# Kernel tuning notes

Measured on AMD Instinct MI355X. Metric: run time of the kernel, lower is better.

The kernel has to match this reference:

```python
import jax, jax.numpy as jnp
import numpy as np

QDEPTH = 20
WIDTH = HEIGHT = 28
PIXELS = WIDTH * HEIGHT          # 784
WIRES = 10                        # ceil(log2(784))
BATCH = 8192


def setup_inputs() -> dict:
    key = jax.random.key(0)
    k1, k2, k3, k4 = jax.random.split(key, 4)
    x = jax.random.normal(k1, (BATCH, 1, WIDTH, HEIGHT), jnp.float32)
    W = jax.random.normal(k2, (WIRES, PIXELS), jnp.float32) / np.sqrt(PIXELS)
    b = jax.random.normal(k3, (WIRES,), jnp.float32) * 0.01
    qweights = jax.random.normal(k4, (QDEPTH, WIRES, 3), jnp.float32) * 0.4
    return {"x": x, "W": W, "b": b, "qweights": qweights}


def _apply_1q(state, gate, wire):
    """Apply a single-qubit gate. state: (B,)+(2,)*WIRES; gate: (2,2) or (B,2,2)."""
    ax = 1 + wire
    s = jnp.moveaxis(state, ax, 1)
    shp = s.shape
    s = s.reshape(shp[0], 2, -1)
    if gate.ndim == 2:
        s = jnp.einsum('ij,bjr->bir', gate, s)
    else:
        s = jnp.einsum('bij,bjr->bir', gate, s)
    return jnp.moveaxis(s.reshape(shp), 1, ax)


def _cnot(state, c, t):
    """CNOT with control c, target t on state (B,)+(2,)*WIRES."""
    s = jnp.moveaxis(state, (1 + c, 1 + t), (1, 2))
    # when control==1, flip target axis
    s = jnp.concatenate([s[:, :1], jnp.flip(s[:, 1:2], axis=2)], axis=1)
    return jnp.moveaxis(s, (1, 2), (1 + c, 1 + t))


def _ry_batched(theta):
    """theta: (B,) -> (B,2,2) complex RY gates."""
    c = jnp.cos(theta / 2)
    s = jnp.sin(theta / 2)
    g = jnp.stack([jnp.stack([c, -s], -1), jnp.stack([s, c], -1)], -2)
    return g.astype(jnp.complex64)


def _rot(phi, theta, omega):
    """PennyLane Rot(phi,theta,omega) = RZ(omega) RY(theta) RZ(phi), scalars -> (2,2)."""
    c = jnp.cos(theta / 2)
    s = jnp.sin(theta / 2)
    m00 = jnp.exp(-0.5j * (phi + omega)) * c
    m01 = -jnp.exp(0.5j * (phi - omega)) * s
    m10 = jnp.exp(-0.5j * (phi - omega)) * s
    m11 = jnp.exp(0.5j * (phi + omega)) * c
    return jnp.stack([jnp.stack([m00, m01]), jnp.stack([m10, m11])]).astype(jnp.complex64)


def _forward(x, W, b, qweights):
    B = x.shape[0]
    feat = x.reshape(B, -1)                       # b 1 w h -> b (w h)
    angles = feat @ W.T + b                       # linear_down -> (B, WIRES)

    # |0...0> statevector, wire 0 most significant (PennyLane convention)
    state = jnp.zeros((B,) + (2,) * WIRES, jnp.complex64)
    state = state.at[(slice(None),) + (0,) * WIRES].set(1.0)

    # AngleEmbedding, rotation='Y'
    for w in range(WIRES):
        state = _apply_1q(state, _ry_batched(angles[:, w]), w)

    # StronglyEntanglingLayers: per-layer Rot on every wire, then CNOT ring
    for l in range(QDEPTH):
        for w in range(WIRES):
            state = _apply_1q(state, _rot(qweights[l, w, 0], qweights[l, w, 1], qweights[l, w, 2]), w)
        r = (l % (WIRES - 1)) + 1                 # default PennyLane ranges
        for w in range(WIRES):
            state = _cnot(state, w, (w + r) % WIRES)

    sv = state.reshape(B, -1)
    probs = sv.real ** 2 + sv.imag ** 2           # qml.probs over all wires
    out = jnp.clip(probs[:, :PIXELS] * PIXELS, 0.0, 1.0)
    return out.reshape(B, 1, WIDTH, HEIGHT)


def reference(x, W, b, qweights):
    return _forward(x, W, b, qweights)
```

## Files before the change

kernel.cpp:

```cpp
#include <hip/hip_runtime.h>
#include <hip/hip_bf16.h>
#include <stdint.h>


#define NWIRES  10
#define DIM     1024
#define NLAYERS 20
#define NGATES  200
#define NPASS   100
#define PIXELS  784
#define BATCH   8192

typedef _Float16 f16;
typedef _Float16 f16x8 __attribute__((ext_vector_type(8)));
typedef float    f32x4 __attribute__((ext_vector_type(4)));
typedef float    f32x2 __attribute__((ext_vector_type(2)));

typedef const __attribute__((address_space(1))) void* gas1_t;
typedef __attribute__((address_space(3))) void*       las3_t;

__device__ __forceinline__ void gload_lds16(const void* g, void* l) {
  __builtin_amdgcn_global_load_lds((gas1_t)g, (las3_t)l, 16, 0, 0);
}

__global__ __launch_bounds__(256) void k_prep(const float* __restrict__ qw,
                                              float* __restrict__ plan_mat,
                                              unsigned* __restrict__ plan_idx,
                                              unsigned* __restrict__ plan_final) {
  __shared__ float gm[NGATES][8];
  const int tid = threadIdx.x;

  if (tid < NGATES) {
    float phi = qw[tid * 3 + 0], th = qw[tid * 3 + 1], om = qw[tid * 3 + 2];
    float s, c, sa, ca, sb, cb;
    sincosf(0.5f * th, &s, &c);
    sincosf(0.5f * (phi + om), &sa, &ca);
    sincosf(0.5f * (phi - om), &sb, &cb);
    gm[tid][0] = ca * c;  gm[tid][1] = sa * c;
    gm[tid][2] = cb * s;  gm[tid][3] = sb * s;
    gm[tid][4] = -cb * s; gm[tid][5] = sb * s;
    gm[tid][6] = ca * c;  gm[tid][7] = -sa * c;
  }
  __syncthreads();

  if (tid == 0) {
    unsigned rowA[NWIRES], invc[NWIRES];
    for (int i = 0; i < NWIRES; i++) { rowA[i] = 1u << i; invc[i] = 1u << i; }
    for (int lrev = 0; lrev < NLAYERS; lrev++) {
      int l = NLAYERS - 1 - lrev;
      int r = (l % (NWIRES - 1)) + 1;
      for (int w = NWIRES - 1; w >= 0; w--) {
        int c = w, t = (w + r) % NWIRES;
        int pc = 9 - c, pt = 9 - t;
        rowA[pt] ^= rowA[pc];
        invc[pc] ^= invc[pt];
      }
      for (int s = 0; s < 5; s++) {
        int w1 = 2 * s, w2 = 2 * s + 1;
        int p1 = 9 - w1, p2 = 9 - w2;
        unsigned u1 = rowA[p1], u2 = rowA[p2];
        unsigned m1 = invc[p1], m2 = invc[p2];
        unsigned b1 = u1 & (0u - u1);
        if (u2 & b1) u2 ^= u1;
        unsigned b2 = u2 & (0u - u2);
        if (u1 & b2) u1 ^= u2;
        unsigned bLo = (b1 < b2) ? b1 : b2;
        unsigned bHi = (b1 < b2) ? b2 : b1;
        unsigned* P = plan_idx + (size_t)(lrev * 5 + s) * 8;
        P[0] = bLo; P[1] = bHi; P[2] = u1; P[3] = u2;
        P[4] = b1;  P[5] = b2;  P[6] = m1; P[7] = m2;
      }
    }
    for (int p = 0; p < NWIRES; p++) plan_final[p] = invc[p];
  } else if (tid >= 100 && tid < 200) {
    int t = tid - 100;
    int lrev = t / 5, s = t % 5;
    int l = NLAYERS - 1 - lrev;
    int g1 = l * NWIRES + 2 * s, g2 = g1 + 1;
    float* K = plan_mat + (size_t)t * 64;
#pragma unroll
    for (int r = 0; r < 4; r++) {
#pragma unroll
      for (int c = 0; c < 4; c++) {
        int r1 = r >> 1, c1 = c >> 1, r2 = r & 1, c2 = c & 1;
        float ar = gm[g1][(r1 * 2 + c1) * 2], ai = gm[g1][(r1 * 2 + c1) * 2 + 1];
        float br = gm[g2][(r2 * 2 + c2) * 2], bi = gm[g2][(r2 * 2 + c2) * 2 + 1];
        float kr = ar * br - ai * bi;
        float ki = ar * bi + ai * br;
        float* e = K + (r * 4 + c) * 4;
        e[0] = kr; e[1] = kr; e[2] = -ki; e[3] = ki;
      }
    }
  }
}

__global__ __launch_bounds__(256) void k_main(const float* __restrict__ plan_mat,
                                              const unsigned* __restrict__ plan_idx,
                                              const unsigned* __restrict__ plan_final,
                                              const float* __restrict__ x,
                                              const float* __restrict__ W,
                                              const float* __restrict__ bias,
                                              f16* __restrict__ E,
                                              f16* __restrict__ Bt) {
  __shared__ f32x2 st[DIM];
  __shared__ float part[4][NWIRES];
  __shared__ float csh[NWIRES][2];

  const int tid = threadIdx.x;

  if (blockIdx.x < PIXELS) {
    const int col = blockIdx.x;

    for (int i = tid; i < DIM; i += 256)
      st[i] = (f32x2){i == col ? 1.f : 0.f, 0.f};
    __syncthreads();

    for (int t = 0; t < NPASS; t++) {
      const unsigned* P = plan_idx + (size_t)t * 8;
      const unsigned bLo = P[0], bHi = P[1], u1 = P[2], u2 = P[3];
      const unsigned pb1 = P[4], pb2 = P[5], m1 = P[6], m2 = P[7];
      const f32x4* Kp = (const f32x4*)(plan_mat + (size_t)t * 64);

      unsigned q  = (unsigned)tid;
      unsigned xx = ((q & ~(bLo - 1u)) << 1) | (q & (bLo - 1u));
      unsigned j0 = ((xx & ~(bHi - 1u)) << 1) | (xx & (bHi - 1u));
      unsigned j  = j0 ^ ((__popc(u1 & j0) & 1) ? pb1 : 0u)
                       ^ ((__popc(u2 & j0) & 1) ? pb2 : 0u);

      f32x2 v0 = st[j];
      f32x2 v1 = st[j ^ m2];
      f32x2 v2 = st[j ^ m1];
      f32x2 v3 = st[j ^ m1 ^ m2];
      f32x2 w0 = {v0.y, v0.x}, w1 = {v1.y, v1.x};
      f32x2 w2 = {v2.y, v2.x}, w3 = {v3.y, v3.x};

      f32x2 r0 = {0.f, 0.f}, r1 = {0.f, 0.f}, r2 = {0.f, 0.f}, r3 = {0.f, 0.f};
#define CM(rr, e, vv, ww)                         \
      { f32x4 kk = Kp[e];                         \
        rr += (f32x2){kk.x, kk.y} * (vv);         \
        rr += (f32x2){kk.z, kk.w} * (ww); }
      CM(r0, 0, v0, w0)  CM(r0, 1, v1, w1)  CM(r0, 2, v2, w2)  CM(r0, 3, v3, w3)
      CM(r1, 4, v0, w0)  CM(r1, 5, v1, w1)  CM(r1, 6, v2, w2)  CM(r1, 7, v3, w3)
      CM(r2, 8, v0, w0)  CM(r2, 9, v1, w1)  CM(r2, 10, v2, w2) CM(r2, 11, v3, w3)
      CM(r3, 12, v0, w0) CM(r3, 13, v1, w1) CM(r3, 14, v2, w2) CM(r3, 15, v3, w3)
#undef CM

      st[j]           = r0;
      st[j ^ m2]      = r1;
      st[j ^ m1]      = r2;
      st[j ^ m1 ^ m2] = r3;
      __syncthreads();
    }

    unsigned invl[NWIRES];
#pragma unroll
    for (int p = 0; p < NWIRES; p++) invl[p] = plan_final[p];

    __align__(8) f16 re4[4], im4[4];
#pragma unroll
    for (int u = 0; u < 4; u++) {
      int i = tid * 4 + u;
      unsigned j = 0;
#pragma unroll
      for (int p = 0; p < NWIRES; p++)
        if ((i >> p) & 1) j ^= invl[p];
      f32x2 v = st[j];
      re4[u] = (f16)v.x;
      im4[u] = (f16)(-v.y);
    }
    *(uint2*)(&Bt[(size_t)(2 * col) * DIM + tid * 4])     = *(const uint2*)re4;
    *(uint2*)(&Bt[(size_t)(2 * col + 1) * DIM + tid * 4]) = *(const uint2*)im4;
    return;
  }

  const int b = blockIdx.x - PIXELS;
  const float* xr = x + (size_t)b * PIXELS;

  float acc[NWIRES];
#pragma unroll
  for (int w = 0; w < NWIRES; w++) acc[w] = 0.f;

  for (int k = tid; k < PIXELS; k += 256) {
    float xv = xr[k];
#pragma unroll
    for (int w = 0; w < NWIRES; w++) acc[w] = fmaf(xv, W[w * PIXELS + k], acc[w]);
  }

#pragma unroll
  for (int w = 0; w < NWIRES; w++) {
    float v = acc[w];
#pragma unroll
    for (int off = 32; off > 0; off >>= 1) v += __shfl_xor(v, off, 64);
    acc[w] = v;
  }

  const int wv = tid >> 6, ln = tid & 63;
  if (ln == 0) {
#pragma unroll
    for (int w = 0; w < NWIRES; w++) part[wv][w] = acc[w];
  }
  __syncthreads();
  if (tid < NWIRES) {
    float a = part[0][tid] + part[1][tid] + part[2][tid] + part[3][tid] + bias[tid];
    float s, c;
    sincosf(0.5f * a, &s, &c);
    csh[tid][0] = c;
    csh[tid][1] = s;
  }
  __syncthreads();

  __align__(8) f16 e4[4];
#pragma unroll
  for (int u = 0; u < 4; u++) {
    int i = tid * 4 + u;
    float pr = 1.f;
#pragma unroll
    for (int w = 0; w < NWIRES; w++) pr *= csh[w][(i >> (9 - w)) & 1];
    e4[u] = (f16)pr;
  }
  *(uint2*)(&E[(size_t)b * DIM + tid * 4]) = *(const uint2*)e4;
}

__global__ __launch_bounds__(512, 2) void k_gemm(const f16* __restrict__ E,
                                                 const f16* __restrict__ Bt,
                                                 float* __restrict__ out) {
  __shared__ __align__(16) f16 As[4][256 * 32];
  __shared__ __align__(16) f16 Bs[4][256 * 32];

  const int tid = threadIdx.x;
  const int wid = tid >> 6, ln = tid & 63;
  const int wm = wid >> 2, wn = wid & 3;

  const int bid = blockIdx.x;
  const int swz = (bid & 7) * 28 + (bid >> 3);
  const int mt  = swz % 32, nt = swz / 32;
  const int m0  = mt * 256;
  const int n0  = nt * 256;

  f32x4 acc[8][4];
#pragma unroll
  for (int a = 0; a < 8; a++)
#pragma unroll
    for (int q = 0; q < 4; q++) acc[a][q] = (f32x4){0.f, 0.f, 0.f, 0.f};

  int offA[8], offB[4];
#pragma unroll
  for (int mi = 0; mi < 8; mi++) {
    int Ra = wm * 128 + mi * 16 + (ln & 15);
    offA[mi] = Ra * 32 + (((ln >> 4) ^ ((Ra >> 1) & 3)) * 8);
  }
#pragma unroll
  for (int ni = 0; ni < 4; ni++) {
    int Rb = wn * 64 + ni * 16 + (ln & 15);
    offB[ni] = Rb * 32 + (((ln >> 4) ^ ((Rb >> 1) & 3)) * 8);
  }

  auto stage = [&](int t) {
    const int sb = t & 3;
#pragma unroll
    for (int r = 0; r < 2; r++) {
      int u   = r * 512 + tid;
      int row = u >> 2;
      int c16 = (u & 3) ^ ((row >> 1) & 3);
      gload_lds16((const char*)E + (size_t)(m0 + row) * 2048 + t * 64 + c16 * 16,
                  (char*)&As[sb][0] + (size_t)u * 16);
    }
#pragma unroll
    for (int r = 0; r < 2; r++) {
      int u   = r * 512 + tid;
      int row = u >> 2;
      int c16 = (u & 3) ^ ((row >> 1) & 3);
      gload_lds16((const char*)Bt + (size_t)(n0 + row) * 2048 + t * 64 + c16 * 16,
                  (char*)&Bs[sb][0] + (size_t)u * 16);
    }
  };

  stage(0);
  stage(1);
  stage(2);
  asm volatile("s_waitcnt vmcnt(8)" ::: "memory");
  __builtin_amdgcn_s_barrier();

#pragma unroll 4
  for (int k = 0; k < 32; k++) {
    const int buf = k & 3;
    f16x8 af[8], bf[4];
#pragma unroll
    for (int mi = 0; mi < 8; mi++) af[mi] = *(const f16x8*)&As[buf][offA[mi]];
#pragma unroll
    for (int ni = 0; ni < 4; ni++) bf[ni] = *(const f16x8*)&Bs[buf][offB[ni]];

    if (k < 29) stage(k + 3);

    __builtin_amdgcn_s_setprio(1);
#pragma unroll
    for (int mi = 0; mi < 8; mi++)
#pragma unroll
      for (int ni = 0; ni < 4; ni++)
        acc[mi][ni] = __builtin_amdgcn_mfma_f32_16x16x32_f16(
            af[mi], bf[ni], acc[mi][ni], 0, 0, 0);
    __builtin_amdgcn_s_setprio(0);

    if (k < 29)       { asm volatile("s_waitcnt vmcnt(8)" ::: "memory"); }
    else if (k == 29) { asm volatile("s_waitcnt vmcnt(4)" ::: "memory"); }
    else if (k == 30) { asm volatile("s_waitcnt vmcnt(0)" ::: "memory"); }
    __builtin_amdgcn_s_barrier();
  }

#pragma unroll
  for (int mi = 0; mi < 8; mi++) {
#pragma unroll
    for (int ni = 0; ni < 4; ni++) {
      int n = n0 + wn * 64 + ni * 16 + (ln & 15);
      int p = n >> 1;
      bool even = (ln & 1) == 0;
#pragma unroll
      for (int r = 0; r < 4; r++) {
        float v = acc[mi][ni][r];
        float o = __shfl_xor(v, 1, 64);
        if (even && p < PIXELS) {
          int m = m0 + wm * 128 + mi * 16 + (ln >> 4) * 4 + r;
          float s2 = (v * v + o * o) * (float)PIXELS;
          out[(size_t)m * PIXELS + p] = fminf(fmaxf(s2, 0.f), 1.f);
        }
      }
    }
  }
}

extern "C" void kernel_launch(void* const* d_in, const int* in_sizes, int n_in,
                              void* d_out, int out_size, void* d_ws, size_t ws_size,
                              hipStream_t stream) {
  const float* x    = (const float*)d_in[0];
  const float* W    = (const float*)d_in[1];
  const float* bias = (const float*)d_in[2];
  const float* qw   = (const float*)d_in[3];
  float* out        = (float*)d_out;

  char* ws = (char*)d_ws;
  f16* E  = (f16*)(ws);
  f16* Bt = (f16*)(ws + (size_t)16 * 1024 * 1024);
  float*    plan_mat   = (float*)(ws + (size_t)20 * 1024 * 1024);
  unsigned* plan_idx   = (unsigned*)(ws + (size_t)20 * 1024 * 1024 + 65536);
  unsigned* plan_final = (unsigned*)(ws + (size_t)20 * 1024 * 1024 + 131072);

  k_prep<<<dim3(1), dim3(256), 0, stream>>>(qw, plan_mat, plan_idx, plan_final);
  k_main<<<dim3(PIXELS + BATCH), dim3(256), 0, stream>>>(plan_mat, plan_idx,
                                                         plan_final, x, W, bias,
                                                         E, Bt);
  k_gemm<<<dim3(224), dim3(512), 0, stream>>>(E, Bt, out);
}
```

Baseline: 130.5 us.

## Simulate unitary columns per wavefront with fused 4-qubit passes and precomputed indices

Measured after the change: 185.4 us. +42.1%, slower.

```diff
diff --git a/kernel.cpp b/kernel.cpp
--- a/kernel.cpp
+++ b/kernel.cpp
@@ -7,9 +7,9 @@
 #define DIM     1024
 #define NLAYERS 20
 #define NGATES  200
-#define NPASS   100
 #define PIXELS  784
 #define BATCH   8192
+#define NUBLK   196
 
 typedef _Float16 f16;
 typedef _Float16 f16x8 __attribute__((ext_vector_type(8)));
@@ -23,11 +23,25 @@
   __builtin_amdgcn_global_load_lds((gas1_t)g, (las3_t)l, 16, 0, 0);
 }
 
+#define CM(rr, kk, vv)                                  \
+  { f32x4 k_ = (kk);                                    \
+    rr += (f32x2){k_.x, k_.y} * (vv);                   \
+    rr += (f32x2){k_.z, k_.w} * (f32x2){(vv).y, (vv).x}; }
+
 __global__ __launch_bounds__(256) void k_prep(const float* __restrict__ qw,
-                                              float* __restrict__ plan_mat,
-                                              unsigned* __restrict__ plan_idx,
+                                              float* __restrict__ pmatF,
+                                              float* __restrict__ pmatS,
+                                              unsigned* __restrict__ maskF,
+                                              unsigned* __restrict__ maskS,
+                                              unsigned* __restrict__ jtF,
+                                              unsigned* __restrict__ jtS,
                                               unsigned* __restrict__ plan_final) {
-  __shared__ float gm[NGATES][8];
+  __shared__ float    gm[NGATES][8];
+  __shared__ unsigned sF[40][4];
+  __shared__ unsigned sS[20][2];
+  __shared__ unsigned bF[40][8];
+  __shared__ unsigned bS[20][8];
+  __shared__ unsigned tmpR[96][8];
   const int tid = threadIdx.x;
 
   if (tid < NGATES) {
@@ -44,40 +58,40 @@
   __syncthreads();
 
   if (tid == 0) {
-    unsigned rowA[NWIRES], invc[NWIRES];
-    for (int i = 0; i < NWIRES; i++) { rowA[i] = 1u << i; invc[i] = 1u << i; }
+    unsigned rA[NWIRES], ic[NWIRES];
+#pragma unroll
+    for (int i = 0; i < NWIRES; i++) { rA[i] = 1u << i; ic[i] = 1u << i; }
+#pragma unroll
     for (int lrev = 0; lrev < NLAYERS; lrev++) {
-      int l = NLAYERS - 1 - lrev;
-      int r = (l % (NWIRES - 1)) + 1;
+      const int l = NLAYERS - 1 - lrev;
+      const int r = (l % (NWIRES - 1)) + 1;
+#pragma unroll
       for (int w = NWIRES - 1; w >= 0; w--) {
-        int c = w, t = (w + r) % NWIRES;
-        int pc = 9 - c, pt = 9 - t;
-        rowA[pt] ^= rowA[pc];
-        invc[pc] ^= invc[pt];
+        const int c = w, t = (w + r) % NWIRES;
+        rA[9 - t] ^= rA[9 - c];
+        ic[9 - c] ^= ic[9 - t];
       }
-      for (int s = 0; s < 5; s++) {
-        int w1 = 2 * s, w2 = 2 * s + 1;
-        int p1 = 9 - w1, p2 = 9 - w2;
-        unsigned u1 = rowA[p1], u2 = rowA[p2];
-        unsigned m1 = invc[p1], m2 = invc[p2];
-        unsigned b1 = u1 & (0u - u1);
-        if (u2 & b1) u2 ^= u1;
-        unsigned b2 = u2 & (0u - u2);
-        if (u1 & b2) u1 ^= u2;
-        unsigned bLo = (b1 < b2) ? b1 : b2;
-        unsigned bHi = (b1 < b2) ? b2 : b1;
-        unsigned* P = plan_idx + (size_t)(lrev * 5 + s) * 8;
-        P[0] = bLo; P[1] = bHi; P[2] = u1; P[3] = u2;
-        P[4] = b1;  P[5] = b2;  P[6] = m1; P[7] = m2;
-      }
-    }
-    for (int p = 0; p < NWIRES; p++) plan_final[p] = invc[p];
+      sF[2 * lrev][0] = rA[9]; sF[2 * lrev][1] = rA[8];
+      sF[2 * lrev][2] = rA[7]; sF[2 * lrev][3] = rA[6];
+      maskF[(2 * lrev) * 4 + 0] = ic[9]; maskF[(2 * lrev) * 4 + 1] = ic[8];
+      maskF[(2 * lrev) * 4 + 2] = ic[7]; maskF[(2 * lrev) * 4 + 3] = ic[6];
+      sF[2 * lrev + 1][0] = rA[5]; sF[2 * lrev + 1][1] = rA[4];
+      sF[2 * lrev + 1][2] = rA[3]; sF[2 * lrev + 1][3] = rA[2];
+      maskF[(2 * lrev + 1) * 4 + 0] = ic[5]; maskF[(2 * lrev + 1) * 4 + 1] = ic[4];
+      maskF[(2 * lrev + 1) * 4 + 2] = ic[3]; maskF[(2 * lrev + 1) * 4 + 3] = ic[2];
+      sS[lrev][0] = rA[1]; sS[lrev][1] = rA[0];
+      maskS[lrev * 2 + 0] = ic[1]; maskS[lrev * 2 + 1] = ic[0];
+    }
+#pragma unroll
+    for (int p = 0; p < NWIRES; p++) plan_final[p] = ic[p];
   } else if (tid >= 100 && tid < 200) {
     int t = tid - 100;
     int lrev = t / 5, s = t % 5;
     int l = NLAYERS - 1 - lrev;
     int g1 = l * NWIRES + 2 * s, g2 = g1 + 1;
-    float* K = plan_mat + (size_t)t * 64;
+    float* K = (s == 4) ? (pmatS + (size_t)lrev * 64)
+                        : (pmatF + (size_t)(2 * lrev + (s >> 1)) * 128 +
+                           (size_t)(s & 1) * 64);
 #pragma unroll
     for (int r = 0; r < 4; r++) {
 #pragma unroll
@@ -92,88 +106,222 @@
       }
     }
   }
+  __syncthreads();
+
+  if (tid < 40) {
+    unsigned u1 = sF[tid][0], u2 = sF[tid][1], u3 = sF[tid][2], u4 = sF[tid][3];
+    unsigned b1, b2, b3, b4;
+    b1 = u1 & (0u - u1);
+    if (u2 & b1) u2 ^= u1; if (u3 & b1) u3 ^= u1; if (u4 & b1) u4 ^= u1;
+    b2 = u2 & (0u - u2);
+    if (u1 & b2) u1 ^= u2; if (u3 & b2) u3 ^= u2; if (u4 & b2) u4 ^= u2;
+    b3 = u3 & (0u - u3);
+    if (u1 & b3) u1 ^= u3; if (u2 & b3) u2 ^= u3; if (u4 & b3) u4 ^= u3;
+    b4 = u4 & (0u - u4);
+    if (u1 & b4) u1 ^= u4; if (u2 & b4) u2 ^= u4; if (u3 & b4) u3 ^= u4;
+    const unsigned piv = b1 | b2 | b3 | b4;
+    unsigned echPack = 0; int cnt = 0, nrem = 0;
+    for (int f = 0; f < NWIRES; f++) {
+      unsigned ef = 1u << f;
+      if (ef & piv) continue;
+      unsigned v = ef ^ (((u1 >> f) & 1u) ? b1 : 0u)
+                      ^ (((u2 >> f) & 1u) ? b2 : 0u)
+                      ^ (((u3 >> f) & 1u) ? b3 : 0u)
+                      ^ (((u4 >> f) & 1u) ? b4 : 0u);
+      unsigned n = v & 15u;
+#pragma unroll
+      for (int rep = 0; rep < 4; rep++) {
+#pragma unroll
+        for (int k2 = 0; k2 < 4; k2++) {
+          unsigned h = (echPack >> (8 * k2)) & 255u;
+          if (h) { unsigned hb = 0x80000000u >> __clz(h); if (n & hb) n ^= h; }
+        }
+      }
+      if (n && cnt < 4) { echPack |= n << (8 * cnt); bF[tid][cnt] = v; cnt++; }
+      else              { tmpR[tid][nrem] = v; nrem++; }
+    }
+    for (int i = 0; i < nrem; i++) bF[tid][cnt + i] = tmpR[tid][i];
+  } else if (tid >= 64 && tid < 84) {
+    const int lr = tid - 64;
+    unsigned u1 = sS[lr][0], u2 = sS[lr][1];
+    unsigned b1 = u1 & (0u - u1);
+    if (u2 & b1) u2 ^= u1;
+    unsigned b2 = u2 & (0u - u2);
+    if (u1 & b2) u1 ^= u2;
+    const unsigned piv = b1 | b2;
+    unsigned echPack = 0; int cnt = 0, nrem = 0;
+    for (int f = 0; f < NWIRES; f++) {
+      unsigned ef = 1u << f;
+      if (ef & piv) continue;
+      unsigned v = ef ^ (((u1 >> f) & 1u) ? b1 : 0u)
+                      ^ (((u2 >> f) & 1u) ? b2 : 0u);
+      unsigned n = v & 15u;
+#pragma unroll
+      for (int rep = 0; rep < 4; rep++) {
+#pragma unroll
+        for (int k2 = 0; k2 < 4; k2++) {
+          unsigned h = (echPack >> (8 * k2)) & 255u;
+          if (h) { unsigned hb = 0x80000000u >> __clz(h); if (n & hb) n ^= h; }
+        }
+      }
+      if (n && cnt < 4) { echPack |= n << (8 * cnt); bS[lr][cnt] = v; cnt++; }
+      else              { tmpR[tid][nrem] = v; nrem++; }
+    }
+    for (int i = 0; i < nrem; i++) bS[lr][cnt + i] = tmpR[tid][i];
+  }
+  __syncthreads();
+
+  for (int e = tid; e < 40 * 64; e += 256) {
+    int fid = e >> 6, l6 = e & 63;
+    unsigned j = 0;
+#pragma unroll
+    for (int b = 0; b < 6; b++)
+      if ((l6 >> b) & 1) j ^= bF[fid][b];
+    jtF[e] = j;
+  }
+  for (int e = tid; e < 20 * 256; e += 256) {
+    int lr = e >> 8, r8 = e & 255;
+    unsigned j = 0;
+#pragma unroll
+    for (int b = 0; b < 8; b++)
+      if ((r8 >> b) & 1) j ^= bS[lr][b];
+    jtS[e] = j;
+  }
 }
 
-__global__ __launch_bounds__(256) void k_main(const float* __restrict__ plan_mat,
-                                              const unsigned* __restrict__ plan_idx,
+__global__ __launch_bounds__(256) void k_main(const float* __restrict__ pmatF,
+                                              const float* __restrict__ pmatS,
+                                              const unsigned* __restrict__ maskF,
+                                              const unsigned* __restrict__ maskS,
+                                              const unsigned* __restrict__ jtF,
+                                              const unsigned* __restrict__ jtS,
                                               const unsigned* __restrict__ plan_final,
                                               const float* __restrict__ x,
                                               const float* __restrict__ W,
                                               const float* __restrict__ bias,
                                               f16* __restrict__ E,
                                               f16* __restrict__ Bt) {
-  __shared__ f32x2 st[DIM];
+  __shared__ f32x2 st4[4][DIM];
   __shared__ float part[4][NWIRES];
   __shared__ float csh[NWIRES][2];
 
   const int tid = threadIdx.x;
-
-  if (blockIdx.x < PIXELS) {
-    const int col = blockIdx.x;
-
-    for (int i = tid; i < DIM; i += 256)
-      st[i] = (f32x2){i == col ? 1.f : 0.f, 0.f};
-    __syncthreads();
-
-    for (int t = 0; t < NPASS; t++) {
-      const unsigned* P = plan_idx + (size_t)t * 8;
-      const unsigned bLo = P[0], bHi = P[1], u1 = P[2], u2 = P[3];
-      const unsigned pb1 = P[4], pb2 = P[5], m1 = P[6], m2 = P[7];
-      const f32x4* Kp = (const f32x4*)(plan_mat + (size_t)t * 64);
-
-      unsigned q  = (unsigned)tid;
-      unsigned xx = ((q & ~(bLo - 1u)) << 1) | (q & (bLo - 1u));
-      unsigned j0 = ((xx & ~(bHi - 1u)) << 1) | (xx & (bHi - 1u));
-      unsigned j  = j0 ^ ((__popc(u1 & j0) & 1) ? pb1 : 0u)
-                       ^ ((__popc(u2 & j0) & 1) ? pb2 : 0u);
-
-      f32x2 v0 = st[j];
-      f32x2 v1 = st[j ^ m2];
-      f32x2 v2 = st[j ^ m1];
-      f32x2 v3 = st[j ^ m1 ^ m2];
-      f32x2 w0 = {v0.y, v0.x}, w1 = {v1.y, v1.x};
-      f32x2 w2 = {v2.y, v2.x}, w3 = {v3.y, v3.x};
-
-      f32x2 r0 = {0.f, 0.f}, r1 = {0.f, 0.f}, r2 = {0.f, 0.f}, r3 = {0.f, 0.f};
-#define CM(rr, e, vv, ww)                         \
-      { f32x4 kk = Kp[e];                         \
-        rr += (f32x2){kk.x, kk.y} * (vv);         \
-        rr += (f32x2){kk.z, kk.w} * (ww); }
-      CM(r0, 0, v0, w0)  CM(r0, 1, v1, w1)  CM(r0, 2, v2, w2)  CM(r0, 3, v3, w3)
-      CM(r1, 4, v0, w0)  CM(r1, 5, v1, w1)  CM(r1, 6, v2, w2)  CM(r1, 7, v3, w3)
-      CM(r2, 8, v0, w0)  CM(r2, 9, v1, w1)  CM(r2, 10, v2, w2) CM(r2, 11, v3, w3)
-      CM(r3, 12, v0, w0) CM(r3, 13, v1, w1) CM(r3, 14, v2, w2) CM(r3, 15, v3, w3)
-#undef CM
-
-      st[j]           = r0;
-      st[j ^ m2]      = r1;
-      st[j ^ m1]      = r2;
-      st[j ^ m1 ^ m2] = r3;
-      __syncthreads();
+  const int wv = tid >> 6, ln = tid & 63;
+
+  if (blockIdx.x < NUBLK) {
+    const int col = blockIdx.x * 4 + wv;
+    f32x2* st = st4[wv];
+
+#pragma unroll
+    for (int i = 0; i < 16; i++) {
+      int idx = ln + 64 * i;
+      st[idx] = (f32x2){idx == col ? 1.f : 0.f, 0.f};
+    }
+    asm volatile("s_waitcnt lgkmcnt(0)" ::: "memory");
+    __builtin_amdgcn_wave_barrier();
+
+    auto FUSED = [&](int fid, unsigned j) {
+      const unsigned mA1 = maskF[fid * 4 + 0], mA2 = maskF[fid * 4 + 1];
+      const unsigned mB1 = maskF[fid * 4 + 2], mB2 = maskF[fid * 4 + 3];
+      const f32x4* Ka = (const f32x4*)(pmatF + (size_t)fid * 128);
+      const f32x4* Kb = Ka + 16;
+      unsigned ra[4], cb[4];
+      ra[0] = j; ra[1] = j ^ mA2; ra[2] = j ^ mA1; ra[3] = j ^ mA1 ^ mA2;
+      cb[0] = 0; cb[1] = mB2;     cb[2] = mB1;     cb[3] = mB1 ^ mB2;
+      f32x2 v[4][4];
+#pragma unroll
+      for (int ia = 0; ia < 4; ia++)
+#pragma unroll
+        for (int ib = 0; ib < 4; ib++)
+          v[ia][ib] = st[ra[ia] ^ cb[ib]];
+      f32x2 u[4][4];
+#pragma unroll
+      for (int ib = 0; ib < 4; ib++)
+#pragma unroll
+        for (int ia = 0; ia < 4; ia++) {
+          f32x2 acc = {0.f, 0.f};
+#pragma unroll
+          for (int ja = 0; ja < 4; ja++) CM(acc, Ka[ia * 4 + ja], v[ja][ib]);
+          u[ia][ib] = acc;
+        }
+#pragma unroll
+      for (int ia = 0; ia < 4; ia++)
+#pragma unroll
+        for (int ib = 0; ib < 4; ib++) {
+          f32x2 acc = {0.f, 0.f};
+#pragma unroll
+          for (int jb = 0; jb < 4; jb++) CM(acc, Kb[ib * 4 + jb], u[ia][jb]);
+          st[ra[ia] ^ cb[ib]] = acc;
+        }
+      asm volatile("s_waitcnt lgkmcnt(0)" ::: "memory");
+      __builtin_amdgcn_wave_barrier();
+    };
+
+    auto SINGLE = [&](int lay, unsigned j0, unsigned j1, unsigned j2,
+                      unsigned j3) {
+      const unsigned m1 = maskS[lay * 2 + 0], m2 = maskS[lay * 2 + 1];
+      const f32x4* Ks = (const f32x4*)(pmatS + (size_t)lay * 64);
+      unsigned js[4] = {j0, j1, j2, j3};
+#pragma unroll
+      for (int q = 0; q < 4; q++) {
+        unsigned j = js[q];
+        f32x2 v0 = st[j], v1 = st[j ^ m2], v2 = st[j ^ m1], v3 = st[j ^ m1 ^ m2];
+        f32x2 r0 = {0.f, 0.f}, r1 = {0.f, 0.f}, r2 = {0.f, 0.f}, r3 = {0.f, 0.f};
+        CM(r0, Ks[0],  v0) CM(r0, Ks[1],  v1) CM(r0, Ks[2],  v2) CM(r0, Ks[3],  v3)
+        CM(r1, Ks[4],  v0) CM(r1, Ks[5],  v1) CM(r1, Ks[6],  v2) CM(r1, Ks[7],  v3)
+        CM(r2, Ks[8],  v0) CM(r2, Ks[9],  v1) CM(r2, Ks[10], v2) CM(r2, Ks[11], v3)
+        CM(r3, Ks[12], v0) CM(r3, Ks[13], v1) CM(r3, Ks[14], v2) CM(r3, Ks[15], v3)
+        st[j]           = r0;
+        st[j ^ m2]      = r1;
+        st[j ^ m1]      = r2;
+        st[j ^ m1 ^ m2] = r3;
+      }
+      asm volatile("s_waitcnt lgkmcnt(0)" ::: "memory");
+      __builtin_amdgcn_wave_barrier();
+    };
+
+    unsigned jFn = jtF[ln];
+    unsigned jS0, jS1, jS2, jS3;
+    for (int lay = 0; lay < NLAYERS; lay++) {
+      unsigned j = jFn;
+      jFn = jtF[(2 * lay + 1) * 64 + ln];
+      FUSED(2 * lay, j);
+      j = jFn;
+      jS0 = jtS[lay * 256 + ln];
+      jS1 = jtS[lay * 256 + ln + 64];
+      jS2 = jtS[lay * 256 + ln + 128];
+      jS3 = jtS[lay * 256 + ln + 192];
+      FUSED(2 * lay + 1, j);
+      if (lay < NLAYERS - 1) jFn = jtF[(2 * lay + 2) * 64 + ln];
+      SINGLE(lay, jS0, jS1, jS2, jS3);
     }
 
     unsigned invl[NWIRES];
 #pragma unroll
     for (int p = 0; p < NWIRES; p++) invl[p] = plan_final[p];
 
-    __align__(8) f16 re4[4], im4[4];
-#pragma unroll
-    for (int u = 0; u < 4; u++) {
-      int i = tid * 4 + u;
+    __align__(16) f16 re16[16], im16[16];
+#pragma unroll
+    for (int u = 0; u < 16; u++) {
+      int i = ln * 16 + u;
       unsigned j = 0;
 #pragma unroll
       for (int p = 0; p < NWIRES; p++)
         if ((i >> p) & 1) j ^= invl[p];
       f32x2 v = st[j];
-      re4[u] = (f16)v.x;
-      im4[u] = (f16)(-v.y);
-    }
-    *(uint2*)(&Bt[(size_t)(2 * col) * DIM + tid * 4])     = *(const uint2*)re4;
-    *(uint2*)(&Bt[(size_t)(2 * col + 1) * DIM + tid * 4]) = *(const uint2*)im4;
+      re16[u] = (f16)v.x;
+      im16[u] = (f16)(-v.y);
+    }
+    uint4* dR = (uint4*)&Bt[(size_t)(2 * col) * DIM + ln * 16];
+    uint4* dI = (uint4*)&Bt[(size_t)(2 * col + 1) * DIM + ln * 16];
+    dR[0] = ((const uint4*)re16)[0];
+    dR[1] = ((const uint4*)re16)[1];
+    dI[0] = ((const uint4*)im16)[0];
+    dI[1] = ((const uint4*)im16)[1];
     return;
   }
 
-  const int b = blockIdx.x - PIXELS;
+  const int b = blockIdx.x - NUBLK;
   const float* xr = x + (size_t)b * PIXELS;
 
   float acc[NWIRES];
@@ -194,7 +342,6 @@
     acc[w] = v;
   }
 
-  const int wv = tid >> 6, ln = tid & 63;
   if (ln == 0) {
 #pragma unroll
     for (int w = 0; w < NWIRES; w++) part[wv][w] = acc[w];
@@ -340,13 +487,20 @@
   char* ws = (char*)d_ws;
   f16* E  = (f16*)(ws);
   f16* Bt = (f16*)(ws + (size_t)16 * 1024 * 1024);
-  float*    plan_mat   = (float*)(ws + (size_t)20 * 1024 * 1024);
-  unsigned* plan_idx   = (unsigned*)(ws + (size_t)20 * 1024 * 1024 + 65536);
-  unsigned* plan_final = (unsigned*)(ws + (size_t)20 * 1024 * 1024 + 131072);
-
-  k_prep<<<dim3(1), dim3(256), 0, stream>>>(qw, plan_mat, plan_idx, plan_final);
-  k_main<<<dim3(PIXELS + BATCH), dim3(256), 0, stream>>>(plan_mat, plan_idx,
-                                                         plan_final, x, W, bias,
-                                                         E, Bt);
+  char* pb = ws + (size_t)20 * 1024 * 1024;
+  float*    pmatF      = (float*)(pb);
+  float*    pmatS      = (float*)(pb + 24576);
+  unsigned* maskF      = (unsigned*)(pb + 32768);
+  unsigned* maskS      = (unsigned*)(pb + 36864);
+  unsigned* jtF        = (unsigned*)(pb + 40960);
+  unsigned* jtS        = (unsigned*)(pb + 53248);
+  unsigned* plan_final = (unsigned*)(pb + 77824);
+
+  k_prep<<<dim3(1), dim3(256), 0, stream>>>(qw, pmatF, pmatS, maskF, maskS,
+                                            jtF, jtS, plan_final);
+  k_main<<<dim3(NUBLK + BATCH), dim3(256), 0, stream>>>(pmatF, pmatS, maskF,
+                                                        maskS, jtF, jtS,
+                                                        plan_final, x, W, bias,
+                                                        E, Bt);
   k_gemm<<<dim3(224), dim3(512), 0, stream>>>(E, Bt, out);
 }
```
